# Kernel tuning notes

Measured on AMD Instinct MI355X. Metric: run time of the kernel, lower is better.

Reference implementation:

```python
import jax, jax.numpy as jnp
import numpy as np

IN_DIM = 32
OUT_DIM = 32
VAR_DIM = 64
BATCH = 16384
KER_DIMS = [1024, 1024, 1024, 1024]
NUM_STEPS = 8  # fixed-step RK4 stand-in for adaptive odeint (tol=1e-4)


def setup_inputs() -> dict:
    key = jax.random.key(0)
    ks = jax.random.split(key, 12)
    x = jax.random.normal(ks[0], (BATCH, IN_DIM), dtype=jnp.float32)
    aug = jnp.ones((BATCH, VAR_DIM - IN_DIM), dtype=jnp.float32)
    dims = [VAR_DIM] + KER_DIMS + [VAR_DIM]
    inp = {"x": x, "aug": aug}
    for i, (d1, d2) in enumerate(zip(dims[:-1], dims[1:])):
        # Linear(d1+1, d2): weight (d2, d1+1), bias (d2,)
        inp[f"W{i}"] = jax.random.normal(ks[1 + 2 * i], (d2, d1 + 1), dtype=jnp.float32) * 0.02
        inp[f"b{i}"] = jax.random.normal(ks[2 + 2 * i], (d2,), dtype=jnp.float32) * 0.02
    return inp


def _odefunc(t, y, Ws, bs):
    # y: [B, VAR_DIM]; per-layer concat of scalar time column, Linear, ReLU (except last)
    out = y
    n = len(Ws)
    for i, (W, b) in enumerate(zip(Ws, bs)):
        z = jnp.concatenate([out, jnp.full((out.shape[0], 1), t, dtype=out.dtype)], axis=1)
        out = z @ W.T + b
        if i < n - 1:
            out = jax.nn.relu(out)
    return out


def _integrate(y0, Ws, bs):
    dt = jnp.float32(1.0 / NUM_STEPS)

    def rk4_step(y, t):
        k1 = _odefunc(t, y, Ws, bs)
        k2 = _odefunc(t + 0.5 * dt, y + 0.5 * dt * k1, Ws, bs)
        k3 = _odefunc(t + 0.5 * dt, y + 0.5 * dt * k2, Ws, bs)
        k4 = _odefunc(t + dt, y + dt * k3, Ws, bs)
        return y + (dt / 6.0) * (k1 + 2.0 * k2 + 2.0 * k3 + k4), None

    ts = jnp.arange(NUM_STEPS, dtype=jnp.float32) * dt
    y1, _ = jax.lax.scan(rk4_step, y0, ts)
    return y1


def reference(x, aug, W0, b0, W1, b1, W2, b2, W3, b3, W4, b4):
    Ws = (W0, W1, W2, W3, W4)
    bs = (b0, b1, b2, b3, b4)
    y0 = jnp.concatenate([x, aug], axis=1)  # [B, VAR_DIM]
    y1 = _integrate(y0, Ws, bs)
    return y1[:, :OUT_DIM]
```

## Files before the change

kernel.cpp:

```cpp
#include <hip/hip_runtime.h>
#include <cstdint>
#include <cstddef>

#define BATCH 16384

typedef float f32x4 __attribute__((ext_vector_type(4)));
typedef _Float16 f16x8 __attribute__((ext_vector_type(8)));

__device__ __forceinline__ unsigned short f2h_bits(float f) {
  _Float16 h = (_Float16)f;
  return __builtin_bit_cast(unsigned short, h);
}

__device__ __forceinline__ void async_cp16(const void* g, void* l) {
  __builtin_amdgcn_global_load_lds(
      (const __attribute__((address_space(1))) unsigned int*)g,
      (__attribute__((address_space(3))) unsigned int*)l, 16, 0, 0);
}

#define PIPE_BAR_3() asm volatile("s_waitcnt vmcnt(3)\n\ts_barrier" ::: "memory")
#define PIPE_BAR_0() asm volatile("s_waitcnt vmcnt(0)\n\ts_barrier" ::: "memory")

template <int BM, int BN, int RT, int CT, int K, int N, bool RELU>
__launch_bounds__(512, 4)
__global__ void gemm_h(const unsigned short* __restrict__ A,
                       const unsigned short* __restrict__ Bw,
                       const float* __restrict__ Wfull,
                       const float* __restrict__ bias,
                       float tval,
                       unsigned short* __restrict__ Ch) {
  constexpr int BK = 32;
  constexpr int NI = K / BK;
  static_assert(NI >= 2, "pipeline needs >=2 stages");
  static_assert((BM * 4 + BN * 4) / 512 == 3, "vmcnt(3) assumes 3 loads/stage");
  static_assert(BM == 4 * RT * 16 && BN == 2 * CT * 16, "4x2 waves");
  __shared__ __align__(16) unsigned short smA[3][BM * BK];
  __shared__ __align__(16) unsigned short smB[3][BN * BK];
  __shared__ float biasLds[BN];

  const int tid = threadIdx.x;
  const int wave = tid >> 6;
  const int lane = tid & 63;
  const int quad = lane >> 4;
  const int r16 = lane & 15;

  const int rowA0 = blockIdx.x * BM;
  const int rowB0 = blockIdx.y * BN;
  const int waveM = wave >> 1;
  const int waveN = wave & 1;

  if (tid < BN) {
    const int col = rowB0 + tid;
    biasLds[tid] = bias[col] + tval * Wfull[(size_t)col * (K + 1) + K];
  }

  auto stage = [&](int k0, int buf) {
#pragma unroll
    for (int i = 0; i < BM * 4 / 512; ++i) {
      const int s = i * 512 + tid;
      const int row = s >> 2;
      const int c = (s & 3) ^ ((row >> 1) & 3);
      const unsigned short* g = A + (size_t)(rowA0 + row) * K + (k0 + c * 8);
      char* l = ((char*)smA[buf]) + (size_t)(i * 512 + (wave << 6)) * 16;
      async_cp16(g, l);
    }
    {
      const int s = tid;
      const int row = s >> 2;
      const int c = (s & 3) ^ ((row >> 1) & 3);
      const unsigned short* g = Bw + (size_t)(rowB0 + row) * K + (k0 + c * 8);
      char* l = ((char*)smB[buf]) + (size_t)((wave << 6)) * 16;
      async_cp16(g, l);
    }
  };

  f32x4 acc[RT][CT];
  const f32x4 zero = {0.f, 0.f, 0.f, 0.f};
#pragma unroll
  for (int i = 0; i < RT; ++i)
#pragma unroll
    for (int j = 0; j < CT; ++j) acc[i][j] = zero;

  auto compute = [&](int buf) {
    const unsigned short* sA = smA[buf];
    const unsigned short* sB = smB[buf];
    f16x8 af[RT], bfr[CT];
#pragma unroll
    for (int nt = 0; nt < CT; ++nt) {
      const int row = waveN * (CT * 16) + nt * 16 + r16;
      const int cp = quad ^ ((row >> 1) & 3);
      bfr[nt] = *(const f16x8*)(sB + row * BK + cp * 8);
    }
#pragma unroll
    for (int mt = 0; mt < RT; ++mt) {
      const int row = waveM * (RT * 16) + mt * 16 + r16;
      const int cp = quad ^ ((row >> 1) & 3);
      af[mt] = *(const f16x8*)(sA + row * BK + cp * 8);
    }
#pragma unroll
    for (int mt = 0; mt < RT; ++mt)
#pragma unroll
      for (int nt = 0; nt < CT; ++nt)
        acc[mt][nt] =
            __builtin_amdgcn_mfma_f32_16x16x32_f16(af[mt], bfr[nt], acc[mt][nt], 0, 0, 0);
  };

  stage(0, 0);
  stage(BK, 1);

#pragma unroll
  for (int kk = 0; kk < NI - 1; ++kk) {
    PIPE_BAR_3();
    if (kk + 2 < NI) stage((kk + 2) * BK, (kk + 2) % 3);
    compute(kk % 3);
  }
  PIPE_BAR_0();
  compute((NI - 1) % 3);

#pragma unroll
  for (int mt = 0; mt < RT; ++mt) {
    const int grow0 = rowA0 + waveM * (RT * 16) + mt * 16 + quad * 4;
#pragma unroll
    for (int nt = 0; nt < CT; ++nt) {
      const int lcol = waveN * (CT * 16) + nt * 16 + r16;
      const int gcol = rowB0 + lcol;
      const float bi = biasLds[lcol];
#pragma unroll
      for (int r = 0; r < 4; ++r) {
        float v = acc[mt][nt][r] + bi;
        if (RELU) v = fmaxf(v, 0.0f);
        Ch[(size_t)(grow0 + r) * N + gcol] = f2h_bits(v);
      }
    }
  }
}

#define SBAR  asm volatile("s_barrier" ::: "memory")
#define MBAR  asm volatile("s_waitcnt lgkmcnt(0)\n\ts_barrier" ::: "memory")
#define VBAR8 asm volatile("s_waitcnt vmcnt(8)\n\ts_barrier" ::: "memory")
#define VBAR0 asm volatile("s_waitcnt vmcnt(0)\n\ts_barrier" ::: "memory")

#define PHASE(sA_, sB_, Q, STAGE_STMT, BND)                                   \
  {                                                                           \
    if ((Q) == 0) {                                                           \
      _Pragma("unroll") for (int nt = 0; nt < 4; ++nt) {                      \
        const int row = wc * 64 + nt * 16 + r16;                              \
        const int sw = row & 7;                                               \
        const unsigned short* bp = (sB_) + row * 64;                          \
        bfr[nt][0] = *(const f16x8*)(bp + ((quad ^ sw) << 3));                \
        bfr[nt][1] = *(const f16x8*)(bp + (((4 + quad) ^ sw) << 3));          \
      }                                                                       \
    }                                                                         \
    f16x8 af0[2], af1[2];                                                     \
    _Pragma("unroll") for (int mi = 0; mi < 2; ++mi) {                        \
      const int row = wr * 128 + ((Q) * 2 + mi) * 16 + r16;                   \
      const int sw = row & 7;                                                 \
      const unsigned short* ap = (sA_) + row * 64;                            \
      af0[mi] = *(const f16x8*)(ap + ((quad ^ sw) << 3));                     \
      af1[mi] = *(const f16x8*)(ap + (((4 + quad) ^ sw) << 3));               \
    }                                                                         \
    MBAR;                                                                     \
    STAGE_STMT;                                                               \
    __builtin_amdgcn_s_setprio(1);                                            \
    _Pragma("unroll") for (int mi = 0; mi < 2; ++mi)                          \
      _Pragma("unroll") for (int nt = 0; nt < 4; ++nt) {                      \
        acc[(Q) * 2 + mi][nt] = __builtin_amdgcn_mfma_f32_16x16x32_f16(       \
            af0[mi], bfr[nt][0], acc[(Q) * 2 + mi][nt], 0, 0, 0);             \
        acc[(Q) * 2 + mi][nt] = __builtin_amdgcn_mfma_f32_16x16x32_f16(       \
            af1[mi], bfr[nt][1], acc[(Q) * 2 + mi][nt], 0, 0, 0);             \
      }                                                                       \
    __builtin_amdgcn_s_setprio(0);                                            \
    BND;                                                                      \
  }

#define TILE(sA_, sB_, STG0, STG1, STG3, BND)  \
  {                                            \
    f16x8 bfr[4][2];                           \
    PHASE(sA_, sB_, 0, STG0, SBAR)             \
    PHASE(sA_, sB_, 1, STG1, SBAR)             \
    PHASE(sA_, sB_, 2, ;, SBAR)                \
    PHASE(sA_, sB_, 3, STG3, BND)              \
  }

__launch_bounds__(512, 2)
__global__ void gemm8(const unsigned short* __restrict__ A,
                      const unsigned short* __restrict__ Bw,
                      const float* __restrict__ Wfull,
                      const float* __restrict__ bias,
                      float tval,
                      unsigned short* __restrict__ Ch) {
  __shared__ __align__(16) unsigned short smA[2][256 * 64];
  __shared__ __align__(16) unsigned short smB[2][256 * 64];
  __shared__ float biasLds[256];

  const int tid = threadIdx.x;
  const int wave = tid >> 6;
  const int lane = tid & 63;
  const int quad = lane >> 4;
  const int r16 = lane & 15;
  const int wr = wave >> 2;
  const int wc = wave & 3;

  const int rowA0 = blockIdx.x * 256;
  const int rowB0 = blockIdx.y * 256;
  const unsigned short* Ag = A + (size_t)rowA0 * 1024;
  const unsigned short* Bg = Bw + (size_t)rowB0 * 1024;

  if (tid < 256) {
    const int col = rowB0 + tid;
    biasLds[tid] = bias[col] + tval * Wfull[(size_t)col * 1025 + 1024];
  }

  auto stg = [&](const unsigned short* gbase, unsigned short* lds, int k0, int half) {
#pragma unroll
    for (int i = 0; i < 2; ++i) {
      const int s = half * 1024 + i * 512 + tid;
      const int row = s >> 3;
      const int c = (s & 7) ^ (row & 7);
      const unsigned short* g = gbase + (size_t)row * 1024 + (k0 + (c << 3));
      char* l = (char*)lds + (size_t)(half * 1024 + i * 512 + (wave << 6)) * 16;
      async_cp16(g, l);
    }
  };

  f32x4 acc[8][4];
  const f32x4 zero = {0.f, 0.f, 0.f, 0.f};
#pragma unroll
  for (int i = 0; i < 8; ++i)
#pragma unroll
    for (int j = 0; j < 4; ++j) acc[i][j] = zero;

  stg(Bg, smB[0], 0, 0);  stg(Bg, smB[0], 0, 1);
  stg(Ag, smA[0], 0, 0);  stg(Ag, smA[0], 0, 1);
  stg(Bg, smB[1], 64, 0); stg(Bg, smB[1], 64, 1);
  stg(Ag, smA[1], 64, 0); stg(Ag, smA[1], 64, 1);
  VBAR8;

  for (int tt = 0; tt < 14; tt += 2) {
    const int kn0 = (tt + 2) * 64;
    const int kn1 = (tt + 3) * 64;
    TILE(smA[0], smB[0],
         stg(Bg, smB[0], kn0, 0),
         stg(Bg, smB[0], kn0, 1),
         (stg(Ag, smA[0], kn0, 0), stg(Ag, smA[0], kn0, 1)),
         VBAR8)
    TILE(smA[1], smB[1],
         stg(Bg, smB[1], kn1, 0),
         stg(Bg, smB[1], kn1, 1),
         (stg(Ag, smA[1], kn1, 0), stg(Ag, smA[1], kn1, 1)),
         VBAR8)
  }
  TILE(smA[0], smB[0], ;, ;, ;, VBAR0)
  TILE(smA[1], smB[1], ;, ;, ;, ;)

#pragma unroll
  for (int mt = 0; mt < 8; ++mt) {
    const int grow0 = rowA0 + wr * 128 + mt * 16 + quad * 4;
#pragma unroll
    for (int nt = 0; nt < 4; ++nt) {
      const int lcol = wc * 64 + nt * 16 + r16;
      const int gcol = rowB0 + lcol;
      const float bi = biasLds[lcol];
#pragma unroll
      for (int r = 0; r < 4; ++r) {
        float v = acc[mt][nt][r] + bi;
        v = fmaxf(v, 0.0f);
        Ch[(size_t)(grow0 + r) * 1024 + gcol] = f2h_bits(v);
      }
    }
  }
}

__launch_bounds__(256, 4)
__global__ void gemm_l4(const unsigned short* __restrict__ A,
                        const unsigned short* __restrict__ Bw,
                        const float* __restrict__ Wfull,
                        const float* __restrict__ bias,
                        float tval,
                        float* __restrict__ y, float* __restrict__ ksum,
                        unsigned short* __restrict__ yh,
                        float* __restrict__ outp, int mode, float dt) {
  constexpr int K = 1024, BK = 32, BM = 32, BN = 64, NI = K / BK;
  __shared__ __align__(16) unsigned short smA[2][BM * BK];
  __shared__ __align__(16) unsigned short smB[2][BN * BK];
  __shared__ float biasLds[BN];

  const int tid = threadIdx.x;
  const int wave = tid >> 6;
  const int lane = tid & 63;
  const int quad = lane >> 4;
  const int r16 = lane & 15;

  const int rowA0 = blockIdx.x * BM;
  const int waveM = wave >> 1;
  const int waveN = wave & 1;

  if (tid < BN) {
    biasLds[tid] = bias[tid] + tval * Wfull[(size_t)tid * (K + 1) + K];
  }

  auto stage = [&](int k0, int buf) {
    if (tid < BM * 4) {
      const int s = tid;
      const int row = s >> 2;
      const int c = (s & 3) ^ ((row >> 1) & 3);
      const unsigned short* g = A + (size_t)(rowA0 + row) * K + (k0 + c * 8);
      char* l = ((char*)smA[buf]) + (size_t)(wave << 6) * 16;
      async_cp16(g, l);
    }
    {
      const int s = tid;
      const int row = s >> 2;
      const int c = (s & 3) ^ ((row >> 1) & 3);
      const unsigned short* g = Bw + (size_t)row * K + (k0 + c * 8);
      char* l = ((char*)smB[buf]) + (size_t)(wave << 6) * 16;
      async_cp16(g, l);
    }
  };

  f32x4 acc[2];
  const f32x4 zero = {0.f, 0.f, 0.f, 0.f};
  acc[0] = zero; acc[1] = zero;

  stage(0, 0);

#pragma unroll 2
  for (int kk = 0; kk < NI; ++kk) {
    __syncthreads();
    if (kk + 1 < NI) stage((kk + 1) * BK, (kk + 1) & 1);

    const unsigned short* sA = smA[kk & 1];
    const unsigned short* sB = smB[kk & 1];
    f16x8 af, bfr[2];
    {
      const int row = waveM * 16 + r16;
      const int cp = quad ^ ((row >> 1) & 3);
      af = *(const f16x8*)(sA + row * BK + cp * 8);
    }
#pragma unroll
    for (int nt = 0; nt < 2; ++nt) {
      const int row = (waveN * 2 + nt) * 16 + r16;
      const int cp = quad ^ ((row >> 1) & 3);
      bfr[nt] = *(const f16x8*)(sB + row * BK + cp * 8);
    }
#pragma unroll
    for (int nt = 0; nt < 2; ++nt)
      acc[nt] = __builtin_amdgcn_mfma_f32_16x16x32_f16(af, bfr[nt], acc[nt], 0, 0, 0);
  }

  const int grow0 = rowA0 + waveM * 16 + quad * 4;
#pragma unroll
  for (int nt = 0; nt < 2; ++nt) {
    const int col = waveN * 32 + nt * 16 + r16;
    const float bi = biasLds[col];
#pragma unroll
    for (int r = 0; r < 4; ++r) {
      const float k = acc[nt][r] + bi;
      const int row = grow0 + r;
      const int idx = row * 64 + col;
      if (mode == 0) {
        ksum[idx] = k;
        yh[idx] = f2h_bits(y[idx] + 0.5f * dt * k);
      } else if (mode == 1) {
        ksum[idx] += 2.f * k;
        yh[idx] = f2h_bits(y[idx] + 0.5f * dt * k);
      } else if (mode == 2) {
        ksum[idx] += 2.f * k;
        yh[idx] = f2h_bits(y[idx] + dt * k);
      } else {
        const float yn = y[idx] + (dt / 6.f) * (ksum[idx] + k);
        y[idx] = yn;
        yh[idx] = f2h_bits(yn);
        if (outp && col < 32) outp[row * 32 + col] = yn;
      }
    }
  }
}

__global__ void conv_w(const float* __restrict__ W, unsigned short* __restrict__ Wh,
                       int N, int K) {
  const int idx = blockIdx.x * 256 + threadIdx.x;
  if (idx < N * K) {
    const int n = idx / K;
    const int k = idx - n * K;
    Wh[idx] = f2h_bits(W[(size_t)n * (K + 1) + k]);
  }
}

__global__ void init_y(const float* __restrict__ x, const float* __restrict__ aug,
                       float* __restrict__ y, unsigned short* __restrict__ yh) {
  const int idx = blockIdx.x * 256 + threadIdx.x;
  const int i = idx >> 6;
  const int j = idx & 63;
  const float v = (j < 32) ? x[i * 32 + j] : aug[i * 32 + (j - 32)];
  y[idx] = v;
  yh[idx] = f2h_bits(v);
}

extern "C" void kernel_launch(void* const* d_in, const int* in_sizes, int n_in,
                              void* d_out, int out_size, void* d_ws, size_t ws_size,
                              hipStream_t stream) {
  const float* x = (const float*)d_in[0];
  const float* aug = (const float*)d_in[1];
  const float* W[5];
  const float* b[5];
  for (int i = 0; i < 5; ++i) {
    W[i] = (const float*)d_in[2 + 2 * i];
    b[i] = (const float*)d_in[3 + 2 * i];
  }

  char* ws = (char*)d_ws;
  auto alloc = [&](size_t bytes) -> char* {
    char* p = ws;
    ws += (bytes + 255) & ~(size_t)255;
    return p;
  };
  float* y = (float*)alloc((size_t)BATCH * 64 * 4);
  unsigned short* yh = (unsigned short*)alloc((size_t)BATCH * 64 * 2);
  unsigned short* h1 = (unsigned short*)alloc((size_t)BATCH * 1024 * 2);
  unsigned short* h2 = (unsigned short*)alloc((size_t)BATCH * 1024 * 2);
  float* ksum = (float*)alloc((size_t)BATCH * 64 * 4);
  const int Kdim[5] = {64, 1024, 1024, 1024, 1024};
  const int Ndim[5] = {1024, 1024, 1024, 1024, 64};
  unsigned short* Wh[5];
  for (int i = 0; i < 5; ++i)
    Wh[i] = (unsigned short*)alloc((size_t)Ndim[i] * Kdim[i] * 2);

  for (int i = 0; i < 5; ++i) {
    const int total = Ndim[i] * Kdim[i];
    conv_w<<<(total + 255) / 256, 256, 0, stream>>>(W[i], Wh[i], Ndim[i], Kdim[i]);
  }
  init_y<<<BATCH * 64 / 256, 256, 0, stream>>>(x, aug, y, yh);

  const float dt = 0.125f;
  float* outp = (float*)d_out;

  auto eval = [&](float t, int mode, float* op) {
    gemm_h<256, 128, 4, 4, 64, 1024, true>
        <<<dim3(BATCH / 256, 1024 / 128), 512, 0, stream>>>(
            yh, Wh[0], W[0], b[0], t, h1);
    unsigned short* src = h1;
    unsigned short* dst = h2;
    for (int L = 1; L <= 3; ++L) {
      gemm8<<<dim3(BATCH / 256, 1024 / 256), 512, 0, stream>>>(
          src, Wh[L], W[L], b[L], t, dst);
      unsigned short* tmp = src; src = dst; dst = tmp;
    }
    gemm_l4<<<dim3(BATCH / 32, 1), 256, 0, stream>>>(
        src, Wh[4], W[4], b[4], t, y, ksum, yh, op, mode, dt);
  };

  for (int s = 0; s < 8; ++s) {
    const float t0 = s * dt;
    eval(t0, 0, nullptr);
    eval(t0 + 0.5f * dt, 1, nullptr);
    eval(t0 + 0.5f * dt, 2, nullptr);
    eval(t0 + dt, 3, (s == 7) ? outp : nullptr);
  }
}
```

Baseline: 4.473 ms.

## Restagger A/B prefetch pipeline, relax LDS waits, and swizzle block order for L2 reuse

Reworks the double-buffered K pipeline in the 1024x1024 GEMM so the A tile for the next step is prefetched one tile ahead and B two tiles ahead. The loads are spread across all four phases, and the vmcnt wait drops from 8 to 4. The full lgkmcnt(0) wait before each phase is replaced by a partial lgkmcnt(8) wait on phase 0 plus a plain barrier, so more LDS reads stay in flight. Block indices are also remapped with a swizzle so that consecutive workgroups share weight tiles and get better L2 locality. The new scheme depends on the wait counts matching the exact issue order, so an off-by-one could read stale LDS data.

```diff
diff --git a/kernel.cpp b/kernel.cpp
--- a/kernel.cpp
+++ b/kernel.cpp
@@ -136,8 +136,7 @@
 }
 
 #define SBAR  asm volatile("s_barrier" ::: "memory")
-#define MBAR  asm volatile("s_waitcnt lgkmcnt(0)\n\ts_barrier" ::: "memory")
-#define VBAR8 asm volatile("s_waitcnt vmcnt(8)\n\ts_barrier" ::: "memory")
+#define VBAR4 asm volatile("s_waitcnt vmcnt(4)\n\ts_barrier" ::: "memory")
 #define VBAR0 asm volatile("s_waitcnt vmcnt(0)\n\ts_barrier" ::: "memory")
 
 #define PHASE(sA_, sB_, Q, STAGE_STMT, BND)                                   \
@@ -159,8 +158,9 @@
       af0[mi] = *(const f16x8*)(ap + ((quad ^ sw) << 3));                     \
       af1[mi] = *(const f16x8*)(ap + (((4 + quad) ^ sw) << 3));               \
     }                                                                         \
-    MBAR;                                                                     \
     STAGE_STMT;                                                               \
+    if ((Q) == 0) asm volatile("s_waitcnt lgkmcnt(8)" ::: "memory");          \
+    SBAR;                                                                     \
     __builtin_amdgcn_s_setprio(1);                                            \
     _Pragma("unroll") for (int mi = 0; mi < 2; ++mi)                          \
       _Pragma("unroll") for (int nt = 0; nt < 4; ++nt) {                      \
@@ -173,13 +173,13 @@
     BND;                                                                      \
   }
 
-#define TILE(sA_, sB_, STG0, STG1, STG3, BND)  \
+#define TILE(sA_, sB_, S0, S1, S2, S3, BND)    \
   {                                            \
     f16x8 bfr[4][2];                           \
-    PHASE(sA_, sB_, 0, STG0, SBAR)             \
-    PHASE(sA_, sB_, 1, STG1, SBAR)             \
-    PHASE(sA_, sB_, 2, ;, SBAR)                \
-    PHASE(sA_, sB_, 3, STG3, BND)              \
+    PHASE(sA_, sB_, 0, S0, SBAR)               \
+    PHASE(sA_, sB_, 1, S1, SBAR)               \
+    PHASE(sA_, sB_, 2, S2, SBAR)               \
+    PHASE(sA_, sB_, 3, S3, BND)                \
   }
 
 __launch_bounds__(512, 2)
@@ -201,8 +201,13 @@
   const int wr = wave >> 2;
   const int wc = wave & 3;
 
-  const int rowA0 = blockIdx.x * 256;
-  const int rowB0 = blockIdx.y * 256;
+  const int orig = blockIdx.y * gridDim.x + blockIdx.x;
+  const int swz = (orig & 7) * 32 + (orig >> 3);
+  const int tx = swz & 63;
+  const int ty = swz >> 6;
+
+  const int rowA0 = tx * 256;
+  const int rowB0 = ty * 256;
   const unsigned short* Ag = A + (size_t)rowA0 * 1024;
   const unsigned short* Bg = Bw + (size_t)rowB0 * 1024;
 
@@ -230,28 +235,34 @@
 #pragma unroll
     for (int j = 0; j < 4; ++j) acc[i][j] = zero;
 
+  stg(Ag, smA[0], 0, 0);  stg(Ag, smA[0], 0, 1);
   stg(Bg, smB[0], 0, 0);  stg(Bg, smB[0], 0, 1);
-  stg(Ag, smA[0], 0, 0);  stg(Ag, smA[0], 0, 1);
   stg(Bg, smB[1], 64, 0); stg(Bg, smB[1], 64, 1);
-  stg(Ag, smA[1], 64, 0); stg(Ag, smA[1], 64, 1);
-  VBAR8;
+  VBAR4;
 
   for (int tt = 0; tt < 14; tt += 2) {
-    const int kn0 = (tt + 2) * 64;
-    const int kn1 = (tt + 3) * 64;
+    const int ka0 = (tt + 1) * 64;
+    const int kb0 = (tt + 2) * 64;
     TILE(smA[0], smB[0],
-         stg(Bg, smB[0], kn0, 0),
-         stg(Bg, smB[0], kn0, 1),
-         (stg(Ag, smA[0], kn0, 0), stg(Ag, smA[0], kn0, 1)),
-         VBAR8)
+         stg(Ag, smA[1], ka0, 0),
+         stg(Ag, smA[1], ka0, 1),
+         stg(Bg, smB[0], kb0, 0),
+         stg(Bg, smB[0], kb0, 1),
+         VBAR4)
+    const int ka1 = (tt + 2) * 64;
+    const int kb1 = (tt + 3) * 64;
     TILE(smA[1], smB[1],
-         stg(Bg, smB[1], kn1, 0),
-         stg(Bg, smB[1], kn1, 1),
-         (stg(Ag, smA[1], kn1, 0), stg(Ag, smA[1], kn1, 1)),
-         VBAR8)
-  }
-  TILE(smA[0], smB[0], ;, ;, ;, VBAR0)
-  TILE(smA[1], smB[1], ;, ;, ;, ;)
+         stg(Ag, smA[0], ka1, 0),
+         stg(Ag, smA[0], ka1, 1),
+         stg(Bg, smB[1], kb1, 0),
+         stg(Bg, smB[1], kb1, 1),
+         VBAR4)
+  }
+  TILE(smA[0], smB[0],
+       stg(Ag, smA[1], 15 * 64, 0),
+       stg(Ag, smA[1], 15 * 64, 1),
+       ;, ;, VBAR0)
+  TILE(smA[1], smB[1], ;, ;, ;, ;, ;)
 
 #pragma unroll
   for (int mt = 0; mt < 8; ++mt) {
```

After: 5.113 ms. 1.14x slower.
